# Performance work log

Hardware: AMD Instinct MI355X
Metric: run time of the kernel (lower is better)

## Reference

```python
import jax, jax.numpy as jnp
import numpy as np

CW = 32            # correlationWidth (number of disparities)
HR = 3             # horizontalCorrelationRadius
VR = 3             # verticalCorrelationRadius
EPS = 1e-09        # normalizationEpsilon
KH, KW = 2 * VR + 1, 2 * HR + 1  # unfold kernel (7,7)

B, C, H, W = 2, 16, 128, 256


def _unfold_patches(img):
    # img: [b,c,h,w] -> [b, c*KH*KW, h, w'] ('same' padding, like nn.Unfold with padding=(3,3)).
    # Feature-dim ordering differs from torch's unfold but NCC is invariant to it
    # (mean / norm / dot all reduce over the full patch dim).
    return jax.lax.conv_general_dilated_patches(
        img, (KH, KW), (1, 1), [(VR, VR), (HR, HR)])


def _normalize_patches(p):
    # zero-mean, unit-L2 per patch (reduce over feature dim 1)
    p = p - p.mean(axis=1, keepdims=True)
    return p / jnp.sqrt(jnp.sum(p * p, axis=1, keepdims=True) + EPS)


def setup_inputs() -> dict:
    key = jax.random.key(0)
    k1, k2 = jax.random.split(key)
    im_left = jax.random.normal(k1, (B, C, H, W), dtype=jnp.float32)
    im_right = jax.random.normal(k2, (B, C, H, W), dtype=jnp.float32)
    return {"im_left": im_left, "im_right": im_right}


def reference(im_left, im_right):
    b, c, h, w = im_left.shape
    # ZeroPad2d((0, CW-1, 0, 0)): pad right edge of width by CW-1 zeros
    left_ext = jnp.pad(im_left, ((0, 0), (0, 0), (0, 0), (0, CW - 1)))
    pl = _normalize_patches(_unfold_patches(left_ext))   # [b,P,h,w+CW-1]
    pr = _normalize_patches(_unfold_patches(im_right))   # [b,P,h,w]
    # cost[b,y,x,d] = <normalized left patch at (y, x+d), normalized right patch at (y, x)>
    cost = jnp.stack(
        [jnp.einsum('bpyx,bpyx->byx', pl[..., d:d + w], pr) for d in range(CW)],
        axis=-1)  # [b,h,w,CW]
    return cost
```

## Files before the change

### kernel.cpp

```cpp
#include <hip/hip_runtime.h>

#define NB 2
#define NC 16
#define NH 128
#define NW 256
#define NCW 32
#define HW (NH*NW)
#define PATCH_INV (1.0f/784.0f)
#define EPS_N 1e-9f
#define HB_W 272

__global__ __launch_bounds__(512) void ncc_kernel(
    const float* __restrict__ L, const float* __restrict__ R, float* __restrict__ out)
{
    __shared__ float csL[NW], cs2L[NW], csR[NW], cs2R[NW];
    __shared__ float sSL[288], sInvL[288], sSR[NW], sInvR[NW];
    __shared__ float hbuf[NCW][HB_W];

    const int bid = blockIdx.x;
    const int lin = (bid & 7) * 32 + (bid >> 3);
    const int b = lin >> 7;
    const int y = lin & 127;

    const int t  = threadIdx.x;
    const int dq = t >> 6;
    const int xg = t & 63;
    const int x0 = xg << 2;
    const int d0 = dq << 2;
    const int s  = x0 + d0;

    const size_t base = (size_t)b * NC * HW;

    {
        const float* img = (t < 256) ? L : R;
        const int col = t & 255;
        float a = 0.f, a2 = 0.f;
        #pragma unroll
        for (int dy = -3; dy <= 3; ++dy) {
            int yy = y + dy;
            if ((unsigned)yy < NH) {
                const float* p = img + base + (size_t)yy * NW + col;
                #pragma unroll
                for (int c = 0; c < NC; ++c) {
                    float v = p[c * HW];
                    a += v; a2 += v * v;
                }
            }
        }
        if (t < 256) { csL[col] = a; cs2L[col] = a2; }
        else         { csR[col] = a; cs2R[col] = a2; }
    }
    __syncthreads();

    if (t < 288) {
        float S = 0.f, S2 = 0.f;
        #pragma unroll
        for (int dx = -3; dx <= 3; ++dx) {
            int xx = t + dx;
            if ((unsigned)xx < NW) { S += csL[xx]; S2 += cs2L[xx]; }
        }
        sSL[t]   = S;
        sInvL[t] = rsqrtf(S2 - S * S * PATCH_INV + EPS_N);
    }
    if (t >= 256) {
        const int xr = t - 256;
        float S = 0.f, S2 = 0.f;
        #pragma unroll
        for (int dx = -3; dx <= 3; ++dx) {
            int xx = xr + dx;
            if ((unsigned)xx < NW) { S += csR[xx]; S2 += cs2R[xx]; }
        }
        sSR[xr]   = S;
        sInvR[xr] = rsqrtf(S2 - S * S * PATCH_INV + EPS_N);
    }
    __syncthreads();

    float vp[4][4];
    #pragma unroll
    for (int i = 0; i < 4; ++i)
        #pragma unroll
        for (int j = 0; j < 4; ++j) vp[i][j] = 0.f;

    #pragma unroll
    for (int dy = -3; dy <= 3; ++dy) {
        const int yy = y + dy;
        if ((unsigned)yy < NH) {
            const float* lrow = L + base + (size_t)yy * NW;
            const float* rrow = R + base + (size_t)yy * NW;
            #pragma unroll
            for (int c = 0; c < NC; ++c) {
                const float* lc = lrow + (size_t)c * HW;
                const float* rc = rrow + (size_t)c * HW;
                float4 rv4 = *(const float4*)(rc + x0);
                float rv[4] = {rv4.x, rv4.y, rv4.z, rv4.w};
                float lw[8];
                #pragma unroll
                for (int ch = 0; ch < 2; ++ch) {
                    int col  = s + ch * 4;
                    int colc = col < (NW - 4) ? col : (NW - 4);
                    float4 lv = *(const float4*)(lc + colc);
                    bool ok = (col < NW);
                    lw[ch*4+0] = ok ? lv.x : 0.f;
                    lw[ch*4+1] = ok ? lv.y : 0.f;
                    lw[ch*4+2] = ok ? lv.z : 0.f;
                    lw[ch*4+3] = ok ? lv.w : 0.f;
                }
                #pragma unroll
                for (int xx = 0; xx < 4; ++xx)
                    #pragma unroll
                    for (int j = 0; j < 4; ++j)
                        vp[xx][j] += lw[xx + j] * rv[xx];
            }
        }
    }
    #pragma unroll
    for (int j = 0; j < 4; ++j)
        *(float4*)&hbuf[d0 + j][4 + x0] =
            make_float4(vp[0][j], vp[1][j], vp[2][j], vp[3][j]);
    if (t < 128) {
        int r = t >> 2, q = t & 3;
        int col = (q == 0) ? 0 : (260 + 4 * (q - 1));
        *(float4*)&hbuf[r][col] = make_float4(0.f, 0.f, 0.f, 0.f);
    }
    __syncthreads();

    float res[4][4];
    #pragma unroll
    for (int j = 0; j < 4; ++j) {
        float4 w0 = *(float4*)&hbuf[d0+j][x0];
        float4 w1 = *(float4*)&hbuf[d0+j][x0+4];
        float4 w2 = *(float4*)&hbuf[d0+j][x0+8];
        float w[12] = {w0.x,w0.y,w0.z,w0.w, w1.x,w1.y,w1.z,w1.w, w2.x,w2.y,w2.z,w2.w};
        #pragma unroll
        for (int xx = 0; xx < 4; ++xx) {
            float sum = 0.f;
            #pragma unroll
            for (int k = 1; k <= 7; ++k) sum += w[xx + k];
            float slv = sSL[s + xx + j];
            float ilv = sInvL[s + xx + j];
            float srv = sSR[x0 + xx];
            float irv = sInvR[x0 + xx];
            res[xx][j] = (sum - slv * srv * PATCH_INV) * ilv * irv;
        }
    }

    float* op = out + (((size_t)(b * NH + y) * NW) + x0) * NCW + d0;
    #pragma unroll
    for (int xx = 0; xx < 4; ++xx)
        *(float4*)(op + (size_t)xx * NCW) =
            make_float4(res[xx][0], res[xx][1], res[xx][2], res[xx][3]);
}

extern "C" void kernel_launch(void* const* d_in, const int* in_sizes, int n_in,
                              void* d_out, int out_size, void* d_ws, size_t ws_size,
                              hipStream_t stream) {
    const float* L = (const float*)d_in[0];
    const float* R = (const float*)d_in[1];
    float* out = (float*)d_out;
    ncc_kernel<<<dim3(NB * NH), dim3(512), 0, stream>>>(L, R, out);
}
```

Baseline: 87.08 us.

## Split each row into two half-width strips with halo recomputation

Each block now handles half of an image row (128 columns) with 256 threads instead of a full row with 512 threads, which doubles the grid to 512 blocks. Column-sum and window-sum stages are resized to cover each strip plus its halo. The horizontal box-filter halo columns at the strip edges are recomputed directly from global memory by extra threads. The aim is more blocks per device and better occupancy, at the cost of redundant halo work and an extra serial per-element halo loop.

```diff
diff --git a/kernel.cpp b/kernel.cpp
--- a/kernel.cpp
+++ b/kernel.cpp
@@ -8,70 +8,78 @@
 #define HW (NH*NW)
 #define PATCH_INV (1.0f/784.0f)
 #define EPS_N 1e-9f
-#define HB_W 272
 
-__global__ __launch_bounds__(512) void ncc_kernel(
+#define SW  128
+#define LCS 165
+#define RCS 134
+#define NSL 159
+#define NSR 128
+#define HBS 136
+
+__global__ __launch_bounds__(256, 2) void ncc_kernel(
     const float* __restrict__ L, const float* __restrict__ R, float* __restrict__ out)
 {
-    __shared__ float csL[NW], cs2L[NW], csR[NW], cs2R[NW];
-    __shared__ float sSL[288], sInvL[288], sSR[NW], sInvR[NW];
-    __shared__ float hbuf[NCW][HB_W];
+    __shared__ float csL[LCS], cs2L[LCS], csR[RCS], cs2R[RCS];
+    __shared__ float sSL[NSL + 1], sInvL[NSL + 1], sSR[NSR], sInvR[NSR];
+    __shared__ float hbuf[NCW][HBS];
 
     const int bid = blockIdx.x;
-    const int lin = (bid & 7) * 32 + (bid >> 3);
-    const int b = lin >> 7;
-    const int y = lin & 127;
+    const int lin = (bid & 7) * 64 + (bid >> 3);
+    const int b   = lin >> 8;
+    const int rr  = lin & 255;
+    const int y   = rr >> 1;
+    const int st  = rr & 1;
+    const int x0s = st * SW;
 
     const int t  = threadIdx.x;
-    const int dq = t >> 6;
-    const int xg = t & 63;
-    const int x0 = xg << 2;
-    const int d0 = dq << 2;
+    const int dg = t >> 5;
+    const int xg = t & 31;
+    const int x0 = x0s + (xg << 2);
+    const int d0 = dg << 2;
     const int s  = x0 + d0;
 
     const size_t base = (size_t)b * NC * HW;
 
-    {
-        const float* img = (t < 256) ? L : R;
-        const int col = t & 255;
+    for (int j = t; j < LCS + RCS; j += 256) {
+        const bool isL = j < LCS;
+        const int lcl = isL ? j : (j - LCS);
+        const int g = x0s - 3 + lcl;
         float a = 0.f, a2 = 0.f;
-        #pragma unroll
-        for (int dy = -3; dy <= 3; ++dy) {
-            int yy = y + dy;
-            if ((unsigned)yy < NH) {
-                const float* p = img + base + (size_t)yy * NW + col;
-                #pragma unroll
-                for (int c = 0; c < NC; ++c) {
-                    float v = p[c * HW];
-                    a += v; a2 += v * v;
+        if ((unsigned)g < NW) {
+            const float* img = isL ? L : R;
+            #pragma unroll
+            for (int dy = -3; dy <= 3; ++dy) {
+                const int yy = y + dy;
+                if ((unsigned)yy < NH) {
+                    const float* p = img + base + (size_t)yy * NW + g;
+                    #pragma unroll
+                    for (int c = 0; c < NC; ++c) {
+                        float v = p[c * HW];
+                        a += v; a2 += v * v;
+                    }
                 }
             }
         }
-        if (t < 256) { csL[col] = a; cs2L[col] = a2; }
-        else         { csR[col] = a; cs2R[col] = a2; }
+        if (isL) { csL[lcl] = a; cs2L[lcl] = a2; }
+        else     { csR[lcl] = a; cs2R[lcl] = a2; }
     }
     __syncthreads();
 
-    if (t < 288) {
-        float S = 0.f, S2 = 0.f;
-        #pragma unroll
-        for (int dx = -3; dx <= 3; ++dx) {
-            int xx = t + dx;
-            if ((unsigned)xx < NW) { S += csL[xx]; S2 += cs2L[xx]; }
+    for (int j = t; j < NSL + NSR; j += 256) {
+        if (j < NSL) {
+            float S = 0.f, S2 = 0.f;
+            #pragma unroll
+            for (int k = 0; k < 7; ++k) { S += csL[j + k]; S2 += cs2L[j + k]; }
+            sSL[j]   = S;
+            sInvL[j] = rsqrtf(S2 - S * S * PATCH_INV + EPS_N);
+        } else {
+            const int xr = j - NSL;
+            float S = 0.f, S2 = 0.f;
+            #pragma unroll
+            for (int k = 0; k < 7; ++k) { S += csR[xr + k]; S2 += cs2R[xr + k]; }
+            sSR[xr]   = S;
+            sInvR[xr] = rsqrtf(S2 - S * S * PATCH_INV + EPS_N);
         }
-        sSL[t]   = S;
-        sInvL[t] = rsqrtf(S2 - S * S * PATCH_INV + EPS_N);
-    }
-    if (t >= 256) {
-        const int xr = t - 256;
-        float S = 0.f, S2 = 0.f;
-        #pragma unroll
-        for (int dx = -3; dx <= 3; ++dx) {
-            int xx = xr + dx;
-            if ((unsigned)xx < NW) { S += csR[xx]; S2 += cs2R[xx]; }
-        }
-        sSR[xr]   = S;
-        sInvR[xr] = rsqrtf(S2 - S * S * PATCH_INV + EPS_N);
     }
     __syncthreads();
 
@@ -115,32 +123,52 @@
     }
     #pragma unroll
     for (int j = 0; j < 4; ++j)
-        *(float4*)&hbuf[d0 + j][4 + x0] =
+        *(float4*)&hbuf[d0 + j][4 + (xg << 2)] =
             make_float4(vp[0][j], vp[1][j], vp[2][j], vp[3][j]);
-    if (t < 128) {
-        int r = t >> 2, q = t & 3;
-        int col = (q == 0) ? 0 : (260 + 4 * (q - 1));
-        *(float4*)&hbuf[r][col] = make_float4(0.f, 0.f, 0.f, 0.f);
+
+    if (t < 192) {
+        const int hi = t >> 5;
+        const int d  = t & 31;
+        const int rel = (hi < 3) ? (hi - 3) : (125 + hi);
+        const int gr = x0s + rel;
+        const int gl = gr + d;
+        float acc = 0.f;
+        if ((unsigned)gr < NW) {
+            const bool lok = gl < NW;
+            const int gla = lok ? gl : 0;
+            #pragma unroll
+            for (int dy = -3; dy <= 3; ++dy) {
+                const int yy = y + dy;
+                if ((unsigned)yy < NH) {
+                    const float* lrow = L + base + (size_t)yy * NW;
+                    const float* rrow = R + base + (size_t)yy * NW;
+                    #pragma unroll
+                    for (int c = 0; c < NC; ++c) {
+                        float lv = lrow[(size_t)c * HW + gla];
+                        lv = lok ? lv : 0.f;
+                        acc += lv * rrow[(size_t)c * HW + gr];
+                    }
+                }
+            }
+        }
+        hbuf[d][4 + rel] = acc;
     }
     __syncthreads();
 
     float res[4][4];
     #pragma unroll
     for (int j = 0; j < 4; ++j) {
-        float4 w0 = *(float4*)&hbuf[d0+j][x0];
-        float4 w1 = *(float4*)&hbuf[d0+j][x0+4];
-        float4 w2 = *(float4*)&hbuf[d0+j][x0+8];
-        float w[12] = {w0.x,w0.y,w0.z,w0.w, w1.x,w1.y,w1.z,w1.w, w2.x,w2.y,w2.z,w2.w};
+        float w[10];
+        #pragma unroll
+        for (int k = 0; k < 10; ++k) w[k] = hbuf[d0 + j][(xg << 2) + 1 + k];
         #pragma unroll
         for (int xx = 0; xx < 4; ++xx) {
             float sum = 0.f;
             #pragma unroll
-            for (int k = 1; k <= 7; ++k) sum += w[xx + k];
-            float slv = sSL[s + xx + j];
-            float ilv = sInvL[s + xx + j];
-            float srv = sSR[x0 + xx];
-            float irv = sInvR[x0 + xx];
-            res[xx][j] = (sum - slv * srv * PATCH_INV) * ilv * irv;
+            for (int k = 0; k < 7; ++k) sum += w[xx + k];
+            const int xel = (xg << 2) + xx + d0 + j;
+            const int xrl = (xg << 2) + xx;
+            res[xx][j] = (sum - sSL[xel] * sSR[xrl] * PATCH_INV) * sInvL[xel] * sInvR[xrl];
         }
     }
 
@@ -157,5 +185,5 @@
     const float* L = (const float*)d_in[0];
     const float* R = (const float*)d_in[1];
     float* out = (float*)d_out;
-    ncc_kernel<<<dim3(NB * NH), dim3(512), 0, stream>>>(L, R, out);
+    ncc_kernel<<<dim3(NB * NH * 2), dim3(256), 0, stream>>>(L, R, out);
 }
```

Measured after the change: 95.40 us. 9.6% more time.
